# Performance work log

Hardware: AMD Instinct MI355X
Metric: run time of the kernel (lower is better)

Reference implementation:

```python
import jax, jax.numpy as jnp
import numpy as np

B, V, H = 16384, 1024, 256


def setup_inputs() -> dict:
    key = jax.random.key(0)
    k1, k2 = jax.random.split(key)
    # binary spin configurations in {0,1}
    batch = jax.random.bernoulli(k1, 0.5, (B, V)).astype(jnp.float32)
    # small weights + negative hidden bias keep exp(log p*) finite in fp32
    weights_amp = jax.random.normal(k2, (H, V), dtype=jnp.float32) * (0.05 / np.sqrt(V))
    visible_bias_amp = jnp.zeros((V,), dtype=jnp.float32)
    hidden_bias_amp = -5.0 * jnp.ones((H,), dtype=jnp.float32)
    return {
        'batch': batch,
        'weights_amp': weights_amp,
        'visible_bias_amp': visible_bias_amp,
        'hidden_bias_amp': hidden_bias_amp,
        'k': 8,
    }


def _gibbs_sampling_amp(v0, W, vb, hb, k, key):
    """k steps of block Gibbs sampling, vectorized over the whole batch [B,V]."""
    keys = jax.random.split(key, 2 * k).reshape(k, 2)

    def step(v, ks):
        ph = jax.nn.sigmoid(v @ W.T + hb)                      # [B,H]
        h = (jax.random.uniform(ks[0], ph.shape) < ph).astype(v.dtype)
        pv = jax.nn.sigmoid(h @ W + vb)                        # [B,V]
        v = (jax.random.uniform(ks[1], pv.shape) < pv).astype(v.dtype)
        return v, None

    vk, _ = jax.lax.scan(step, v0, keys)
    return vk


def reference(batch, weights_amp, visible_bias_amp, hidden_bias_amp, k):
    W, vb, hb = weights_amp, visible_bias_amp, hidden_bias_amp
    nbatch = batch.shape[0]
    key = jax.random.key(42)

    vk = _gibbs_sampling_amp(batch, W, vb, hb, k, key)          # [B,V]

    ph0 = jax.nn.sigmoid(batch @ W.T + hb)                      # [B,H] positive-phase hidden probs
    pre_k = vk @ W.T + hb                                       # [B,H]
    phk = jax.nn.sigmoid(pre_k)                                 # [B,H] negative-phase hidden probs

    # unnormalized_probability_amp(vk) = exp(vk.vb + sum_j softplus((W vk + hb)_j))
    log_p = vk @ vb + jax.nn.softplus(pre_k).sum(axis=-1)       # [B]
    inv_norm = jnp.exp(-log_p) / nbatch                         # 1 / (len(batch) * p*(vk))

    # g_W = sum_b [outer(phk_b, vk_b) - outer(ph0_b, v0_b)] / norm_b
    g_w = (jnp.einsum('b,bh,bv->hv', inv_norm, phk, vk)
           - jnp.einsum('b,bh,bv->hv', inv_norm, ph0, batch))   # [H,V]
    g_vb = jnp.einsum('b,bv->v', inv_norm, vk - batch)          # [V]
    g_hb = jnp.einsum('b,bh->h', inv_norm, phk - ph0)           # [H]

    return jnp.concatenate([g_w.ravel(), g_vb, g_hb])
```

## Files before the change

### kernel.cpp

```cpp
#include <hip/hip_runtime.h>
#include <stdint.h>

#define B_DIM 16384
#define V_DIM 1024
#define H_DIM 256
#define K_STEPS 8
#define HALF_B 8192

typedef short bf16x8 __attribute__((ext_vector_type(8)));
typedef float f32x4 __attribute__((ext_vector_type(4)));

__host__ __device__ inline uint32_t rotl32(uint32_t v, int r) {
#if defined(__HIP_DEVICE_COMPILE__)
    return __builtin_amdgcn_alignbit(v, v, (uint32_t)(32 - r));
#else
    return (v << r) | (v >> (32 - r));
#endif
}

__host__ __device__ inline void threefry2x32(uint32_t k0, uint32_t k1,
                                             uint32_t x0, uint32_t x1,
                                             uint32_t* o0, uint32_t* o1) {
    uint32_t k2 = k0 ^ k1 ^ 0x1BD11BDAu;
    x0 += k0; x1 += k1;
#define TF_RND(r) { x0 += x1; x1 = rotl32(x1, (r)); x1 ^= x0; }
    TF_RND(13) TF_RND(15) TF_RND(26) TF_RND(6)
    x0 += k1; x1 += k2 + 1u;
    TF_RND(17) TF_RND(29) TF_RND(16) TF_RND(24)
    x0 += k2; x1 += k0 + 2u;
    TF_RND(13) TF_RND(15) TF_RND(26) TF_RND(6)
    x0 += k0; x1 += k1 + 3u;
    TF_RND(17) TF_RND(29) TF_RND(16) TF_RND(24)
    x0 += k1; x1 += k2 + 4u;
    TF_RND(13) TF_RND(15) TF_RND(26) TF_RND(6)
    x0 += k2; x1 += k0 + 5u;
#undef TF_RND
    *o0 = x0; *o1 = x1;
}

__device__ inline float tf_uniform(uint32_t key0, uint32_t key1, uint32_t e) {
    uint32_t o0, o1;
    threefry2x32(key0, key1, 0u, e, &o0, &o1);
    uint32_t bits = o0 ^ o1;
    return __uint_as_float((bits >> 9) | 0x3f800000u) - 1.0f;
}

__device__ inline uint16_t bf16_rn(float f) {
    uint32_t u = __float_as_uint(f);
    uint32_t r = u + 0x7FFFu + ((u >> 16) & 1u);
    return (uint16_t)(r >> 16);
}
__device__ inline float bf16_to_f32(uint16_t h) {
    return __uint_as_float(((uint32_t)h) << 16);
}

__device__ inline void gload_lds16(const void* g, void* l) {
    __builtin_amdgcn_global_load_lds((const __attribute__((address_space(1))) uint32_t*)g,
                                     (__attribute__((address_space(3))) uint32_t*)l, 16, 0, 0);
}


__global__ void pack_w_kernel(const float* __restrict__ W,
                              ushort* __restrict__ whp, ushort* __restrict__ wlp) {
    int uid = blockIdx.x * 256 + threadIdx.x;
    int l = uid & 63, s = (uid >> 6) & 1, kc = (uid >> 7) & 15, R = uid >> 11;
    int row = R * 16 + (l & 15);
    int col = kc * 64 + s * 32 + (l >> 4) * 8;
    const float* src = W + (size_t)row * V_DIM + col;
    ushort* dh = whp + (size_t)uid * 8;
    ushort* dl = wlp + (size_t)uid * 8;
#pragma unroll
    for (int e = 0; e < 8; ++e) {
        float w = src[e];
        ushort hi = bf16_rn(w);
        dh[e] = hi;
        dl[e] = bf16_rn(w - bf16_to_f32(hi));
    }
}

__global__ void pack_batch_kernel(const float* __restrict__ batch,
                                  ushort* __restrict__ bp) {
    int uid = blockIdx.x * 256 + threadIdx.x;
    int l = uid & 63, s = (uid >> 6) & 1, kc = (uid >> 7) & 15, R = uid >> 11;
    int row = R * 16 + (l & 15);
    int col = kc * 64 + s * 32 + (l >> 4) * 8;
    const float* src = batch + (size_t)row * V_DIM + col;
    ushort* d = bp + (size_t)uid * 8;
#pragma unroll
    for (int e = 0; e < 8; ++e) d[e] = bf16_rn(src[e]);
}

template <int MODE>
__device__ __forceinline__ void gemm_wave_unit(
    const int m0w, const int n0w,
    const ushort* __restrict__ Ap, const ushort* __restrict__ Bhp,
    const ushort* __restrict__ Blp, const float* __restrict__ bias,
    ushort* __restrict__ out, ushort* __restrict__ out2,
    const uint32_t key0, const uint32_t key1) {
    const int lane = threadIdx.x & 63;
    const int q = lane >> 4;
    const int l15 = lane & 15;

    const ushort* apA = Ap + (size_t)(m0w >> 4) * 16384 + lane * 8;
    const ushort* apBh = Bhp + (size_t)(n0w >> 4) * 16384 + lane * 8;
    const ushort* apBl = Blp + (size_t)(n0w >> 4) * 16384 + lane * 8;

    f32x4 acc[2][2] = {};

#pragma unroll 2
    for (int kc = 0; kc < 16; ++kc) {
#pragma unroll
        for (int s = 0; s < 2; ++s) {
            const int go = kc * 1024 + s * 512;
            bf16x8 af[2], bh[2], bl[2];
#pragma unroll
            for (int i = 0; i < 2; ++i)
                af[i] = *(const bf16x8*)(apA + go + i * 16384);
#pragma unroll
            for (int j = 0; j < 2; ++j) {
                bh[j] = *(const bf16x8*)(apBh + go + j * 16384);
                bl[j] = *(const bf16x8*)(apBl + go + j * 16384);
            }
#pragma unroll
            for (int i = 0; i < 2; ++i)
#pragma unroll
                for (int j = 0; j < 2; ++j) {
                    acc[i][j] = __builtin_amdgcn_mfma_f32_16x16x32_bf16(af[i], bh[j], acc[i][j], 0, 0, 0);
                    acc[i][j] = __builtin_amdgcn_mfma_f32_16x16x32_bf16(af[i], bl[j], acc[i][j], 0, 0, 0);
                }
        }
    }

    const int orow = q * 4;
#pragma unroll
    for (int i = 0; i < 2; ++i) {
#pragma unroll
        for (int j = 0; j < 2; ++j) {
            int col = n0w + j * 16 + l15;
            float bv = bias[col];
#pragma unroll
            for (int r = 0; r < 4; ++r) {
                int row = m0w + i * 16 + orow + r;
                float val = acc[i][j][r] + bv;
                if (MODE == 0) {
                    float E = expf(-val);
                    uint32_t e = (uint32_t)row * (uint32_t)H_DIM + (uint32_t)col;
                    float u = tf_uniform(key0, key1, e);
                    out[(size_t)row * H_DIM + col] = (fmaf(u, E, u) < 1.0f) ? (ushort)0x3F80 : (ushort)0;
                } else if (MODE == 3) {
                    float E = expf(-val);
                    float sg = 1.0f / (1.0f + E);
                    uint32_t e = (uint32_t)row * (uint32_t)H_DIM + (uint32_t)col;
                    float u = tf_uniform(key0, key1, e);
                    out[(size_t)row * H_DIM + col] = (fmaf(u, E, u) < 1.0f) ? (ushort)0x3F80 : (ushort)0;
                    out2[(size_t)row * H_DIM + col] = bf16_rn(sg);
                } else {
                    float sg = 1.0f / (1.0f + expf(-val));
                    out[(size_t)row * H_DIM + col] = bf16_rn(sg);
                }
            }
        }
    }
}

__device__ __forceinline__ void vsample_wave_unit(
    const ushort* __restrict__ h, const float* __restrict__ W,
    const float* __restrict__ vb, ushort* __restrict__ vpack,
    ushort* __restrict__ vrow, int write_row,
    uint32_t key0, uint32_t key1, int row2) {
    const int lane = threadIdx.x & 63;

    float vbr[16];
#pragma unroll
    for (int t = 0; t < 16; ++t) vbr[t] = vb[lane + 64 * t];

#pragma unroll
    for (int rr = 0; rr < 2; ++rr) {
        const int b = row2 + rr;
        ushort4 hv = ((const ushort4*)(h + (size_t)b * H_DIM))[lane];
        unsigned long long masks[4];
        masks[0] = __ballot(hv.x != 0);
        masks[1] = __ballot(hv.y != 0);
        masks[2] = __ballot(hv.z != 0);
        masks[3] = __ballot(hv.w != 0);

        float acc[16];
#pragma unroll
        for (int t = 0; t < 16; ++t) acc[t] = 0.0f;

#pragma unroll
        for (int s = 0; s < 4; ++s) {
            unsigned long long m = masks[s];
            while (m) {
                int l = __ffsll(m) - 1;
                m &= m - 1;
                int j = l * 4 + s;
                const float* wrow = W + (size_t)j * V_DIM + lane;
#pragma unroll
                for (int t = 0; t < 16; ++t) acc[t] += wrow[64 * t];
            }
        }

        const uint32_t ebase = (uint32_t)b * (uint32_t)V_DIM + (uint32_t)lane;
        ushort* vp = vpack + (size_t)(b >> 4) * 16384 + (b & 15) * 8 +
                     ((lane >> 5) & 1) * 512 + ((lane >> 3) & 3) * 128 + (lane & 7);
        ushort* orow = vrow + (size_t)b * V_DIM + lane;
#pragma unroll
        for (int t = 0; t < 16; ++t) {
            float pre = acc[t] + vbr[t];
            float E = expf(-pre);
            float u = tf_uniform(key0, key1, ebase + 64u * (uint32_t)t);
            ushort val = (fmaf(u, E, u) < 1.0f) ? (ushort)0x3F80 : (ushort)0;
            vp[t * 1024] = val;
            if (write_row) orow[64 * t] = val;
        }
    }
}

template <int MODE>
__global__ __launch_bounds__(256, 6) void gemm_only(
    const ushort* __restrict__ Ap, const ushort* __restrict__ Bhp,
    const ushort* __restrict__ Blp, const float* __restrict__ bias,
    ushort* __restrict__ out, ushort* __restrict__ out2,
    uint32_t key0, uint32_t key1, int mbase) {
    const int w = threadIdx.x >> 6;
    const int m0w = mbase + blockIdx.x * 64 + (w & 1) * 32;
    const int n0w = blockIdx.y * 64 + (w >> 1) * 32;
    gemm_wave_unit<MODE>(m0w, n0w, Ap, Bhp, Blp, bias, out, out2, key0, key1);
}

template <int MODE>
__global__ __launch_bounds__(192, 6) void hybrid_step(
    const ushort* __restrict__ Ap, const ushort* __restrict__ Whp,
    const ushort* __restrict__ Wlp, const float* __restrict__ hb,
    ushort* __restrict__ hout, ushort* __restrict__ out2,
    uint32_t gk0, uint32_t gk1, int gemm_mbase,
    const ushort* __restrict__ hprev, const float* __restrict__ Wf,
    const float* __restrict__ vb, ushort* __restrict__ vpack,
    ushort* __restrict__ vrow, int write_row,
    uint32_t vk0, uint32_t vk1, int vs_base) {
    const int bid = blockIdx.x;
    const int w = threadIdx.x >> 6;
    if (w < 2) {
        const int u = bid * 2 + w;
        vsample_wave_unit(hprev, Wf, vb, vpack, vrow, write_row, vk0, vk1,
                          vs_base + u * 2);
    } else {
        const int gm = bid & 255;
        const int gn = bid >> 8;
        gemm_wave_unit<MODE>(gemm_mbase + gm * 32, gn * 32, Ap, Whp, Wlp, hb,
                             hout, out2, gk0, gk1);
    }
}

__global__ __launch_bounds__(256, 4) void mfma_gemm_acc(
    const ushort* __restrict__ A, const ushort* __restrict__ Bt,
    float* __restrict__ out, int N, int K, int k_slice) {
    __shared__ __align__(16) ushort As[64 * 64];
    __shared__ __align__(16) ushort Bs[64 * 64];

    const int tid = threadIdx.x;
    const int lane = tid & 63;
    const int w = tid >> 6;
    const int m0 = blockIdx.x * 64;
    const int n0 = blockIdx.y * 64;
    const int kbase = blockIdx.z * k_slice;

    const int wm = (w & 1) * 32;
    const int wn = (w >> 1) * 32;
    const int q = lane >> 4;
    const int l15 = lane & 15;

    const ushort* asrc[2];
    const ushort* bsrc[2];
#pragma unroll
    for (int i = 0; i < 2; ++i) {
        const int j = w * 2 + i;
        const int row = j * 8 + (lane >> 3);
        const int sl = (lane & 7) ^ (row & 7);
        const size_t off = (size_t)row * K + (sl >> 2) * 32 + (sl & 3) * 8;
        asrc[i] = A + (size_t)m0 * K + off;
        bsrc[i] = Bt + (size_t)n0 * K + off;
    }

    f32x4 acc[2][2] = {};

    for (int kt = 0; kt < k_slice; kt += 64) {
        const int k0 = kbase + kt;
#pragma unroll
        for (int i = 0; i < 2; ++i) {
            gload_lds16(asrc[i] + k0, &As[(w * 2 + i) * 512]);
            gload_lds16(bsrc[i] + k0, &Bs[(w * 2 + i) * 512]);
        }
        __syncthreads();
#pragma unroll
        for (int s = 0; s < 2; ++s) {
            bf16x8 af[2], bf[2];
#pragma unroll
            for (int i = 0; i < 2; ++i) {
                const int ra = wm + i * 16 + l15;
                const int rb = wn + i * 16 + l15;
                af[i] = *(const bf16x8*)((const char*)As + ra * 128 +
                                         (((s * 4 + q) ^ (ra & 7)) * 16));
                bf[i] = *(const bf16x8*)((const char*)Bs + rb * 128 +
                                         (((s * 4 + q) ^ (rb & 7)) * 16));
            }
#pragma unroll
            for (int i = 0; i < 2; ++i)
#pragma unroll
                for (int j = 0; j < 2; ++j)
                    acc[i][j] = __builtin_amdgcn_mfma_f32_16x16x32_bf16(af[i], bf[j], acc[i][j], 0, 0, 0);
        }
        __syncthreads();
    }

    const int orow = q * 4;
#pragma unroll
    for (int i = 0; i < 2; ++i)
#pragma unroll
        for (int j = 0; j < 2; ++j) {
            int col = n0 + wn + j * 16 + l15;
#pragma unroll
            for (int r = 0; r < 4; ++r) {
                int row = m0 + wm + i * 16 + orow + r;
                atomicAdd(&out[(size_t)row * N + col], acc[i][j][r]);
            }
        }
}

__global__ __launch_bounds__(256) void lognorm_kernel(
    const ushort* __restrict__ phk, const ushort* __restrict__ vk,
    const float* __restrict__ vb, float* __restrict__ inv) {
    int b = blockIdx.x;
    int tid = threadIdx.x;
    float p = bf16_to_f32(phk[(size_t)b * H_DIM + tid]);
    float s = -log1pf(-p);
    for (int j = tid; j < V_DIM; j += 256)
        s += bf16_to_f32(vk[(size_t)b * V_DIM + j]) * vb[j];
    for (int off = 32; off > 0; off >>= 1) s += __shfl_down(s, off, 64);
    __shared__ float wsum[4];
    int lane = tid & 63, wid = tid >> 6;
    if (lane == 0) wsum[wid] = s;
    __syncthreads();
    if (tid == 0) {
        float t = wsum[0] + wsum[1] + wsum[2] + wsum[3];
        inv[b] = expf(-t) * (1.0f / 16384.0f);
    }
}

__global__ void build_At(const ushort* __restrict__ P, const float* __restrict__ inv,
                         float sgn, ushort* __restrict__ At) {
    __shared__ float T[64][65];
    int c = threadIdx.x & 63;
    int rb = threadIdx.x >> 6;
    int b0 = blockIdx.x * 64;
    int h0 = blockIdx.y * 64;
    for (int r = rb; r < 64; r += 4) {
        int b = b0 + r;
        T[c][r] = sgn * inv[b] * bf16_to_f32(P[(size_t)b * H_DIM + h0 + c]);
    }
    __syncthreads();
    for (int r = rb; r < 64; r += 4)
        At[(size_t)(h0 + r) * B_DIM + b0 + c] = bf16_rn(T[r][c]);
}

__global__ void build_Bt(const ushort* __restrict__ Sb, const float* __restrict__ Sf,
                         int use_f32, ushort* __restrict__ Bt) {
    __shared__ ushort T[64][65];
    int c = threadIdx.x & 63;
    int rb = threadIdx.x >> 6;
    int b0 = blockIdx.x * 64;
    int v0 = blockIdx.y * 64;
    for (int r = rb; r < 64; r += 4) {
        int b = b0 + r;
        T[c][r] = use_f32 ? bf16_rn(Sf[(size_t)b * V_DIM + v0 + c])
                          : Sb[(size_t)b * V_DIM + v0 + c];
    }
    __syncthreads();
    for (int r = rb; r < 64; r += 4)
        Bt[(size_t)(v0 + r) * B_DIM + b0 + c] = T[r][c];
}

__global__ void gvb_kernel(const ushort* __restrict__ vk, const float* __restrict__ batchf,
                           const float* __restrict__ inv, float* __restrict__ gvb) {
    int col = blockIdx.x * 256 + threadIdx.x;
    int b0 = blockIdx.y * 512;
    float acc = 0.0f;
    for (int r = 0; r < 512; ++r) {
        int b = b0 + r;
        acc += inv[b] * (bf16_to_f32(vk[(size_t)b * V_DIM + col]) -
                         batchf[(size_t)b * V_DIM + col]);
    }
    atomicAdd(&gvb[col], acc);
}

__global__ void ghb_kernel(const ushort* __restrict__ phk, const ushort* __restrict__ ph0,
                           const float* __restrict__ inv, float* __restrict__ ghb) {
    int col = threadIdx.x;
    int b0 = blockIdx.x * 256;
    float acc = 0.0f;
    for (int r = 0; r < 256; ++r) {
        int b = b0 + r;
        acc += inv[b] * (bf16_to_f32(phk[(size_t)b * H_DIM + col]) -
                         bf16_to_f32(ph0[(size_t)b * H_DIM + col]));
    }
    atomicAdd(&ghb[col], acc);
}

extern "C" void kernel_launch(void* const* d_in, const int* in_sizes, int n_in,
                              void* d_out, int out_size, void* d_ws, size_t ws_size,
                              hipStream_t stream) {
    const float* batch = (const float*)d_in[0];
    const float* W = (const float*)d_in[1];
    const float* vb = (const float*)d_in[2];
    const float* hb = (const float*)d_in[3];

    char* base = (char*)d_ws;
    ushort* w_hi_p = (ushort*)(base + 0);
    ushort* w_lo_p = (ushort*)(base + 524288);
    float*  inv    = (float*)(base + 1048576);
    ushort* v_pack = (ushort*)(base + 2097152);
    ushort* Bt     = v_pack;
    ushort* v_row  = (ushort*)(base + 35651584);
    ushort* batch_p = v_row;
    ushort* h_cur  = (ushort*)(base + 69206016);
    ushort* At     = h_cur;
    ushort* ph0b   = (ushort*)(base + 77594624);
    ushort* phkb   = (ushort*)(base + 85983232);

    float* gw  = (float*)d_out;
    float* gvb = gw + (size_t)H_DIM * V_DIM;
    float* ghb = gvb + V_DIM;

    hipMemsetAsync(d_out, 0, (size_t)out_size * sizeof(float), stream);

    uint32_t sk0[16], sk1[16];
    for (int n = 0; n < 16; ++n) threefry2x32(0u, 42u, 0u, (uint32_t)n, &sk0[n], &sk1[n]);

    pack_w_kernel<<<dim3(128), dim3(256), 0, stream>>>(W, w_hi_p, w_lo_p);
    pack_batch_kernel<<<dim3(8192), dim3(256), 0, stream>>>(batch, batch_p);

    const dim3 HYB(2048);
    const dim3 HYBT(192);

    gemm_only<3><<<dim3(128, 4), dim3(256), 0, stream>>>(
        batch_p, w_hi_p, w_lo_p, hb, h_cur, ph0b, sk0[0], sk1[0], 0);

    for (int s = 0; s < K_STEPS; ++s) {
        const int wr = (s == K_STEPS - 1) ? 1 : 0;
        if (s == 0) {
            hybrid_step<3><<<HYB, HYBT, 0, stream>>>(
                batch_p, w_hi_p, w_lo_p, hb, h_cur, ph0b, sk0[0], sk1[0], HALF_B,
                h_cur, W, vb, v_pack, v_row, wr, sk0[1], sk1[1], 0);
        } else {
            hybrid_step<0><<<HYB, HYBT, 0, stream>>>(
                v_pack, w_hi_p, w_lo_p, hb, h_cur, nullptr, sk0[2 * s], sk1[2 * s], HALF_B,
                h_cur, W, vb, v_pack, v_row, wr, sk0[2 * s + 1], sk1[2 * s + 1], 0);
        }
        if (s < K_STEPS - 1) {
            hybrid_step<0><<<HYB, HYBT, 0, stream>>>(
                v_pack, w_hi_p, w_lo_p, hb, h_cur, nullptr, sk0[2 * s + 2], sk1[2 * s + 2], 0,
                h_cur, W, vb, v_pack, v_row, wr, sk0[2 * s + 1], sk1[2 * s + 1], HALF_B);
        } else {
            hybrid_step<1><<<HYB, HYBT, 0, stream>>>(
                v_pack, w_hi_p, w_lo_p, hb, phkb, nullptr, 0u, 0u, 0,
                h_cur, W, vb, v_pack, v_row, wr, sk0[2 * s + 1], sk1[2 * s + 1], HALF_B);
        }
    }
    gemm_only<1><<<dim3(128, 4), dim3(256), 0, stream>>>(
        v_pack, w_hi_p, w_lo_p, hb, phkb, nullptr, 0u, 0u, HALF_B);

    lognorm_kernel<<<dim3(B_DIM), dim3(256), 0, stream>>>(phkb, v_row, vb, inv);
    ghb_kernel<<<dim3(B_DIM / 256), dim3(256), 0, stream>>>(phkb, ph0b, inv, ghb);
    gvb_kernel<<<dim3(V_DIM / 256, B_DIM / 512), dim3(256), 0, stream>>>(v_row, batch, inv, gvb);

    build_At<<<dim3(B_DIM / 64, H_DIM / 64), dim3(256), 0, stream>>>(phkb, inv, 1.0f, At);
    build_Bt<<<dim3(B_DIM / 64, V_DIM / 64), dim3(256), 0, stream>>>(v_row, nullptr, 0, Bt);
    mfma_gemm_acc<<<dim3(H_DIM / 64, V_DIM / 64, 16), dim3(256), 0, stream>>>(
        At, Bt, gw, V_DIM, B_DIM, 1024);
    build_At<<<dim3(B_DIM / 64, H_DIM / 64), dim3(256), 0, stream>>>(ph0b, inv, -1.0f, At);
    build_Bt<<<dim3(B_DIM / 64, V_DIM / 64), dim3(256), 0, stream>>>(nullptr, batch, 1, Bt);
    mfma_gemm_acc<<<dim3(H_DIM / 64, V_DIM / 64, 16), dim3(256), 0, stream>>>(
        At, Bt, gw, V_DIM, B_DIM, 1024);
}
```

Baseline: 883.7 us.

## Replace hybrid half-batch overlapped kernels with separate full-batch GEMM and v-sample kernels

Removes the hybrid kernel that ran the sparse v-sampling on one half of the batch while MFMA GEMM waves handled the other half. Each Gibbs step now launches a full-batch gemm_only followed by a dedicated vsample_kernel with 256-thread blocks. The v-sampling epilogue is also regrouped so four exps and RNG draws are computed before their stores, to expose more ILP. This drops the cross-half overlap in exchange for simpler launches and better per-kernel occupancy, and it reduces the launch count.

```diff
diff --git a/kernel.cpp b/kernel.cpp
--- a/kernel.cpp
+++ b/kernel.cpp
@@ -5,7 +5,6 @@
 #define V_DIM 1024
 #define H_DIM 256
 #define K_STEPS 8
-#define HALF_B 8192
 
 typedef short bf16x8 __attribute__((ext_vector_type(8)));
 typedef float f32x4 __attribute__((ext_vector_type(4)));
@@ -163,20 +162,34 @@
     }
 }
 
-__device__ __forceinline__ void vsample_wave_unit(
+template <int MODE>
+__global__ __launch_bounds__(256, 6) void gemm_only(
+    const ushort* __restrict__ Ap, const ushort* __restrict__ Bhp,
+    const ushort* __restrict__ Blp, const float* __restrict__ bias,
+    ushort* __restrict__ out, ushort* __restrict__ out2,
+    uint32_t key0, uint32_t key1) {
+    const int w = threadIdx.x >> 6;
+    const int m0w = blockIdx.x * 64 + (w & 1) * 32;
+    const int n0w = blockIdx.y * 64 + (w >> 1) * 32;
+    gemm_wave_unit<MODE>(m0w, n0w, Ap, Bhp, Blp, bias, out, out2, key0, key1);
+}
+
+__global__ __launch_bounds__(256, 8) void vsample_kernel(
     const ushort* __restrict__ h, const float* __restrict__ W,
     const float* __restrict__ vb, ushort* __restrict__ vpack,
     ushort* __restrict__ vrow, int write_row,
-    uint32_t key0, uint32_t key1, int row2) {
+    uint32_t key0, uint32_t key1) {
     const int lane = threadIdx.x & 63;
+    const int wid = threadIdx.x >> 6;
 
     float vbr[16];
 #pragma unroll
     for (int t = 0; t < 16; ++t) vbr[t] = vb[lane + 64 * t];
 
+    const int row_base = blockIdx.x * 8 + wid * 2;
 #pragma unroll
     for (int rr = 0; rr < 2; ++rr) {
-        const int b = row2 + rr;
+        const int b = row_base + rr;
         ushort4 hv = ((const ushort4*)(h + (size_t)b * H_DIM))[lane];
         unsigned long long masks[4];
         masks[0] = __ballot(hv.x != 0);
@@ -206,50 +219,23 @@
                      ((lane >> 5) & 1) * 512 + ((lane >> 3) & 3) * 128 + (lane & 7);
         ushort* orow = vrow + (size_t)b * V_DIM + lane;
 #pragma unroll
-        for (int t = 0; t < 16; ++t) {
-            float pre = acc[t] + vbr[t];
-            float E = expf(-pre);
-            float u = tf_uniform(key0, key1, ebase + 64u * (uint32_t)t);
-            ushort val = (fmaf(u, E, u) < 1.0f) ? (ushort)0x3F80 : (ushort)0;
-            vp[t * 1024] = val;
-            if (write_row) orow[64 * t] = val;
-        }
-    }
-}
-
-template <int MODE>
-__global__ __launch_bounds__(256, 6) void gemm_only(
-    const ushort* __restrict__ Ap, const ushort* __restrict__ Bhp,
-    const ushort* __restrict__ Blp, const float* __restrict__ bias,
-    ushort* __restrict__ out, ushort* __restrict__ out2,
-    uint32_t key0, uint32_t key1, int mbase) {
-    const int w = threadIdx.x >> 6;
-    const int m0w = mbase + blockIdx.x * 64 + (w & 1) * 32;
-    const int n0w = blockIdx.y * 64 + (w >> 1) * 32;
-    gemm_wave_unit<MODE>(m0w, n0w, Ap, Bhp, Blp, bias, out, out2, key0, key1);
-}
-
-template <int MODE>
-__global__ __launch_bounds__(192, 6) void hybrid_step(
-    const ushort* __restrict__ Ap, const ushort* __restrict__ Whp,
-    const ushort* __restrict__ Wlp, const float* __restrict__ hb,
-    ushort* __restrict__ hout, ushort* __restrict__ out2,
-    uint32_t gk0, uint32_t gk1, int gemm_mbase,
-    const ushort* __restrict__ hprev, const float* __restrict__ Wf,
-    const float* __restrict__ vb, ushort* __restrict__ vpack,
-    ushort* __restrict__ vrow, int write_row,
-    uint32_t vk0, uint32_t vk1, int vs_base) {
-    const int bid = blockIdx.x;
-    const int w = threadIdx.x >> 6;
-    if (w < 2) {
-        const int u = bid * 2 + w;
-        vsample_wave_unit(hprev, Wf, vb, vpack, vrow, write_row, vk0, vk1,
-                          vs_base + u * 2);
-    } else {
-        const int gm = bid & 255;
-        const int gn = bid >> 8;
-        gemm_wave_unit<MODE>(gemm_mbase + gm * 32, gn * 32, Ap, Whp, Wlp, hb,
-                             hout, out2, gk0, gk1);
+        for (int tb = 0; tb < 4; ++tb) {
+            float E[4], u[4];
+#pragma unroll
+            for (int jj = 0; jj < 4; ++jj) {
+                const int t = tb * 4 + jj;
+                float pre = acc[t] + vbr[t];
+                E[jj] = expf(-pre);
+                u[jj] = tf_uniform(key0, key1, ebase + 64u * (uint32_t)t);
+            }
+#pragma unroll
+            for (int jj = 0; jj < 4; ++jj) {
+                const int t = tb * 4 + jj;
+                ushort val = (fmaf(u[jj], E[jj], u[jj]) < 1.0f) ? (ushort)0x3F80 : (ushort)0;
+                vp[t * 1024] = val;
+                if (write_row) orow[64 * t] = val;
+            }
+        }
     }
 }
 
@@ -440,35 +426,23 @@
     pack_w_kernel<<<dim3(128), dim3(256), 0, stream>>>(W, w_hi_p, w_lo_p);
     pack_batch_kernel<<<dim3(8192), dim3(256), 0, stream>>>(batch, batch_p);
 
-    const dim3 HYB(2048);
-    const dim3 HYBT(192);
-
-    gemm_only<3><<<dim3(128, 4), dim3(256), 0, stream>>>(
-        batch_p, w_hi_p, w_lo_p, hb, h_cur, ph0b, sk0[0], sk1[0], 0);
+    const dim3 GGRID(B_DIM / 64, H_DIM / 64);
+    const dim3 VGRID(B_DIM / 8);
 
     for (int s = 0; s < K_STEPS; ++s) {
+        if (s == 0) {
+            gemm_only<3><<<GGRID, dim3(256), 0, stream>>>(
+                batch_p, w_hi_p, w_lo_p, hb, h_cur, ph0b, sk0[0], sk1[0]);
+        } else {
+            gemm_only<0><<<GGRID, dim3(256), 0, stream>>>(
+                v_pack, w_hi_p, w_lo_p, hb, h_cur, nullptr, sk0[2 * s], sk1[2 * s]);
+        }
         const int wr = (s == K_STEPS - 1) ? 1 : 0;
-        if (s == 0) {
-            hybrid_step<3><<<HYB, HYBT, 0, stream>>>(
-                batch_p, w_hi_p, w_lo_p, hb, h_cur, ph0b, sk0[0], sk1[0], HALF_B,
-                h_cur, W, vb, v_pack, v_row, wr, sk0[1], sk1[1], 0);
-        } else {
-            hybrid_step<0><<<HYB, HYBT, 0, stream>>>(
-                v_pack, w_hi_p, w_lo_p, hb, h_cur, nullptr, sk0[2 * s], sk1[2 * s], HALF_B,
-                h_cur, W, vb, v_pack, v_row, wr, sk0[2 * s + 1], sk1[2 * s + 1], 0);
-        }
-        if (s < K_STEPS - 1) {
-            hybrid_step<0><<<HYB, HYBT, 0, stream>>>(
-                v_pack, w_hi_p, w_lo_p, hb, h_cur, nullptr, sk0[2 * s + 2], sk1[2 * s + 2], 0,
-                h_cur, W, vb, v_pack, v_row, wr, sk0[2 * s + 1], sk1[2 * s + 1], HALF_B);
-        } else {
-            hybrid_step<1><<<HYB, HYBT, 0, stream>>>(
-                v_pack, w_hi_p, w_lo_p, hb, phkb, nullptr, 0u, 0u, 0,
-                h_cur, W, vb, v_pack, v_row, wr, sk0[2 * s + 1], sk1[2 * s + 1], HALF_B);
-        }
-    }
-    gemm_only<1><<<dim3(128, 4), dim3(256), 0, stream>>>(
-        v_pack, w_hi_p, w_lo_p, hb, phkb, nullptr, 0u, 0u, HALF_B);
+        vsample_kernel<<<VGRID, dim3(256), 0, stream>>>(
+            h_cur, W, vb, v_pack, v_row, wr, sk0[2 * s + 1], sk1[2 * s + 1]);
+    }
+    gemm_only<1><<<GGRID, dim3(256), 0, stream>>>(
+        v_pack, w_hi_p, w_lo_p, hb, phkb, nullptr, 0u, 0u);
 
     lognorm_kernel<<<dim3(B_DIM), dim3(256), 0, stream>>>(phkb, v_row, vb, inv);
     ghb_kernel<<<dim3(B_DIM / 256), dim3(256), 0, stream>>>(phkb, ph0b, inv, ghb);
```

New measurement: 928.2 us. 5.0% more time.
